# Optimization experiments

Hardware: AMD Instinct MI355X
Metric: run time of the kernel (lower is better)

## Reference

```python
import jax, jax.numpy as jnp
import numpy as np

N_RAYS = 65536
S_UNIFORM = 256          # 2 * n_samples coarse samples per ray
N_IMP = 128              # importance samples per ray
TRUNCATION = 2.0 / 512.0 * 4.0  # default in sdf2weights


def raw2weights_occupancy(raw):
    # raw2outputs_nerf_color with occupancy=True
    alpha = jax.nn.sigmoid(10.0 * raw)  # [N, S]
    trans = jnp.cumprod(
        jnp.concatenate([jnp.ones_like(alpha[:, :1]), 1.0 - alpha + 1e-10], axis=-1),
        axis=-1,
    )[:, :-1]
    return alpha, alpha * trans


def sample_pdf_det(bins, weights, n_samples):
    # bins: [N, M], weights: [N, M-1]; deterministic (det=True) inverse-CDF sampling
    w = weights + 1e-5
    pdf = w / jnp.sum(w, axis=-1, keepdims=True)
    cdf = jnp.cumsum(pdf, axis=-1)
    cdf = jnp.concatenate([jnp.zeros_like(cdf[..., :1]), cdf], axis=-1)  # [N, M]
    u = jnp.linspace(0.0, 1.0, n_samples, dtype=cdf.dtype)
    u = jnp.broadcast_to(u, cdf.shape[:-1] + (n_samples,))               # [N, n]
    inds = jax.vmap(lambda c, uu: jnp.searchsorted(c, uu, side='right'))(cdf, u)
    below = jnp.maximum(inds - 1, 0)
    above = jnp.minimum(inds, cdf.shape[-1] - 1)
    cdf_b = jnp.take_along_axis(cdf, below, axis=-1)
    cdf_a = jnp.take_along_axis(cdf, above, axis=-1)
    bins_b = jnp.take_along_axis(bins, below, axis=-1)
    bins_a = jnp.take_along_axis(bins, above, axis=-1)
    denom = cdf_a - cdf_b
    denom = jnp.where(denom < 1e-5, jnp.ones_like(denom), denom)
    t = (u - cdf_b) / denom
    return bins_b + t * (bins_a - bins_b)


def sdf2weights(sdf, z_vals, truncation=TRUNCATION, sc_factor=1.0):
    alpha = jax.nn.sigmoid(sdf / truncation) * jax.nn.sigmoid(-sdf / truncation)
    signs = sdf[:, 1:] * sdf[:, :-1]
    sign_mask = jnp.where(signs < 0.0, 1.0, 0.0)
    inds = jnp.argmax(sign_mask, axis=1)[:, None]              # first zero-crossing
    z_min = jnp.take_along_axis(z_vals, inds, axis=1)          # [N, 1]
    trunc_mask = jnp.where(z_vals < z_min + sc_factor * truncation, 1.0, 0.0)
    alpha = alpha * trunc_mask
    weights = alpha / (jnp.sum(alpha, axis=-1, keepdims=True) + 1e-8)
    return weights


def setup_inputs() -> dict:
    key = jax.random.key(0)
    k1, k2, k3, k4 = jax.random.split(key, 4)
    occ = jax.random.normal(k1, (N_RAYS, S_UNIFORM), dtype=jnp.float32)
    # monotonically increasing depths in [0.1, 4.1)
    z_vals_u = jnp.sort(
        jax.random.uniform(k2, (N_RAYS, S_UNIFORM), dtype=jnp.float32) * 4.0 + 0.1,
        axis=-1,
    )
    sdf = jax.random.normal(k3, (N_RAYS, N_IMP), dtype=jnp.float32) * 0.05
    rgbs = jax.random.uniform(k4, (N_RAYS, N_IMP, 3), dtype=jnp.float32)
    return {"occ": occ, "z_vals_u": z_vals_u, "sdf": sdf, "rgbs": rgbs}


def reference(occ, z_vals_u, sdf, rgbs):
    # 1) coarse occupancy compositing -> weights
    _, w_u = raw2weights_occupancy(occ)
    # 2) inverse-CDF importance sampling over midpoints (detached, as in gen_samples)
    z_mid = 0.5 * (z_vals_u[..., 1:] + z_vals_u[..., :-1])
    z_samples = jax.lax.stop_gradient(sample_pdf_det(z_mid, w_u[..., 1:-1], N_IMP))
    # 3) TSDF weights at importance samples
    weights = sdf2weights(sdf, z_samples)
    # 4) composite
    rgb_map = jnp.clip(jnp.sum(weights[..., None] * rgbs, axis=-2), 0.0, 1.0)  # [N,3]
    depth_map = jnp.sum(weights * z_samples, axis=-1)                          # [N]
    return jnp.concatenate([rgb_map, depth_map[:, None], weights], axis=-1)    # [N, 4+N_IMP]
```

## Files before the change

### kernel.cpp

```cpp
#include <hip/hip_runtime.h>

#define S_U 256
#define N_IMP 128
#define OUT_STRIDE (4 + N_IMP)
#define TRUNC 0.015625f
#define WPB 4

__device__ __forceinline__ float inv_cdf_sample(const float* __restrict__ cdf,
                                                const float* __restrict__ zm,
                                                float u) {
    int lo = 0, hi = 255;
#pragma unroll
    for (int it = 0; it < 8; ++it) {
        int mid = (lo + hi) >> 1;
        bool c = cdf[mid] <= u;
        lo = c ? mid + 1 : lo;
        hi = c ? hi : mid;
    }
    int below = max(lo - 1, 0);
    int above = min(lo, 254);
    float cb = cdf[below], ca = cdf[above];
    float zb = zm[below],  za = zm[above];
    float denom = ca - cb;
    denom = (denom < 1e-5f) ? 1.0f : denom;
    float t = (u - cb) / denom;
    return zb + t * (za - zb);
}

__global__ __launch_bounds__(256) void tsdf_render_kernel(
    const float* __restrict__ occ,
    const float* __restrict__ zvals,
    const float* __restrict__ sdf,
    const float* __restrict__ rgbs,
    float* __restrict__ out)
{
    const int lane = threadIdx.x & 63;
    const int wv   = threadIdx.x >> 6;
    const int ray  = blockIdx.x * WPB + wv;

    __shared__ __align__(16) float s_cdf [WPB][S_U];
    __shared__ __align__(16) float s_zmid[WPB][S_U];

    const float4 o4 = ((const float4*)(occ   + (size_t)ray * S_U))[lane];
    const float4 z4 = ((const float4*)(zvals + (size_t)ray * S_U))[lane];

    float a0 = 1.0f / (1.0f + __expf(-10.0f * o4.x));
    float a1 = 1.0f / (1.0f + __expf(-10.0f * o4.y));
    float a2 = 1.0f / (1.0f + __expf(-10.0f * o4.z));
    float a3 = 1.0f / (1.0f + __expf(-10.0f * o4.w));
    float t0 = 1.0f - a0 + 1e-10f;
    float t1 = 1.0f - a1 + 1e-10f;
    float t2 = 1.0f - a2 + 1e-10f;
    float t3 = 1.0f - a3 + 1e-10f;

    float pp0 = t0, pp1 = pp0 * t1, pp2 = pp1 * t2, pp3 = pp2 * t3;
    float ip = pp3;
#pragma unroll
    for (int d = 1; d < 64; d <<= 1) {
        float y = __shfl_up(ip, d);
        if (lane >= d) ip *= y;
    }
    float pbase = __shfl_up(ip, 1);
    if (lane == 0) pbase = 1.0f;

    float w0 = a0 * pbase;
    float w1 = a1 * pbase * pp0;
    float w2 = a2 * pbase * pp1;
    float w3 = a3 * pbase * pp2;

    float v0 = (lane > 0)  ? w0 + 1e-5f : 0.0f;
    float v1 = w1 + 1e-5f;
    float v2 = w2 + 1e-5f;
    float v3 = (lane < 63) ? w3 + 1e-5f : 0.0f;
    float s0 = v0, s1 = s0 + v1, s2 = s1 + v2, s3 = s2 + v3;
    float is = s3;
#pragma unroll
    for (int d = 1; d < 64; d <<= 1) {
        float y = __shfl_up(is, d);
        if (lane >= d) is += y;
    }
    float total = __shfl(is, 63);
    float sbase = __shfl_up(is, 1);
    if (lane == 0) sbase = 0.0f;
    float invt = 1.0f / total;

    float4 cdf4;
    cdf4.x = (sbase + s0) * invt;
    cdf4.y = (sbase + s1) * invt;
    cdf4.z = (sbase + s2) * invt;
    cdf4.w = (sbase + s3) * invt;
    *((float4*)&s_cdf[wv][lane * 4]) = cdf4;

    float znext = __shfl_down(z4.x, 1);
    float4 zm4;
    zm4.x = 0.5f * (z4.x + z4.y);
    zm4.y = 0.5f * (z4.y + z4.z);
    zm4.z = 0.5f * (z4.z + z4.w);
    zm4.w = 0.5f * (z4.w + znext);
    *((float4*)&s_zmid[wv][lane * 4]) = zm4;

    __builtin_amdgcn_wave_barrier();

    const float2 sd2 = ((const float2*)(sdf + (size_t)ray * N_IMP))[lane];
    const float2* rg = (const float2*)(rgbs + (size_t)ray * (N_IMP * 3)) + lane * 3;
    float2 p0 = rg[0];
    float2 p1 = rg[1];
    float2 p2 = rg[2];

    const float* cdfp = s_cdf[wv];
    const float* zmp  = s_zmid[wv];
    float u0 = (float)(2 * lane)     * (1.0f / 127.0f);
    float u1 = (float)(2 * lane + 1) * (1.0f / 127.0f);
    float zs0 = inv_cdf_sample(cdfp, zmp, u0);
    float zs1 = inv_cdf_sample(cdfp, zmp, u1);

    float sn = __shfl_down(sd2.x, 1);
    int c = 0x7fffffff;
    if (sd2.x * sd2.y < 0.0f)                     c = 2 * lane;
    else if (lane < 63 && sd2.y * sn < 0.0f)      c = 2 * lane + 1;
#pragma unroll
    for (int d = 32; d > 0; d >>= 1) c = min(c, __shfl_xor(c, d));
    int ci = (c == 0x7fffffff) ? 0 : c;
    float zca = __shfl(zs0, ci >> 1);
    float zcb = __shfl(zs1, ci >> 1);
    float z_min = (ci & 1) ? zcb : zca;

    float x0 = sd2.x * (1.0f / TRUNC);
    float x1 = sd2.y * (1.0f / TRUNC);
    float al0 = 1.0f / (2.0f + __expf(x0) + __expf(-x0));
    float al1 = 1.0f / (2.0f + __expf(x1) + __expf(-x1));
    float zlim = z_min + TRUNC;
    if (!(zs0 < zlim)) al0 = 0.0f;
    if (!(zs1 < zlim)) al1 = 0.0f;

    float asum = al0 + al1;
#pragma unroll
    for (int d = 32; d > 0; d >>= 1) asum += __shfl_xor(asum, d);
    float inv_s = 1.0f / (asum + 1e-8f);
    float g0 = al0 * inv_s;
    float g1 = al1 * inv_s;

    float rr = g0 * p0.x + g1 * p1.y;
    float gg = g0 * p0.y + g1 * p2.x;
    float bb = g0 * p1.x + g1 * p2.y;
    float dd = g0 * zs0  + g1 * zs1;
#pragma unroll
    for (int d = 32; d > 0; d >>= 1) {
        rr += __shfl_xor(rr, d);
        gg += __shfl_xor(gg, d);
        bb += __shfl_xor(bb, d);
        dd += __shfl_xor(dd, d);
    }

    float* ob = out + (size_t)ray * OUT_STRIDE;
    ((float2*)(ob + 4))[lane] = make_float2(g0, g1);
    if (lane == 0) {
        ob[0] = fminf(fmaxf(rr, 0.0f), 1.0f);
        ob[1] = fminf(fmaxf(gg, 0.0f), 1.0f);
        ob[2] = fminf(fmaxf(bb, 0.0f), 1.0f);
        ob[3] = dd;
    }
}

extern "C" void kernel_launch(void* const* d_in, const int* in_sizes, int n_in,
                              void* d_out, int out_size, void* d_ws, size_t ws_size,
                              hipStream_t stream) {
    const float* occ  = (const float*)d_in[0];
    const float* z    = (const float*)d_in[1];
    const float* sdf  = (const float*)d_in[2];
    const float* rgbs = (const float*)d_in[3];
    float* out = (float*)d_out;
    const int n_rays = in_sizes[0] / S_U;
    hipLaunchKernelGGL(tsdf_render_kernel, dim3(n_rays / WPB), dim3(256), 0, stream,
                       occ, z, sdf, rgbs, out);
}
```

Baseline: 263.6 us.

## Replace binary-search inverse CDF with scatter-based bucket lookup and DPP scans

Each lane computes which uniform sample indices its CDF entries bracket and scatters the 'below' index into shared memory. This replaces the per-sample 8-step binary search over LDS with a direct lookup. CDF and midpoint values are interleaved as float2 pairs so the below/above fetches pair up. Shuffle-based scans and reductions are replaced with DPP row operations. The colour and depth sums are reduced before normalisation, and the sdf/rgb loads are hoisted to the kernel start to overlap latency. The risks are the exactness of k_of at bucket boundaries and divergent scatter loops when the CDF is steep.

```diff
diff --git a/kernel.cpp b/kernel.cpp
--- a/kernel.cpp
+++ b/kernel.cpp
@@ -5,26 +5,51 @@
 #define OUT_STRIDE (4 + N_IMP)
 #define TRUNC 0.015625f
 #define WPB 4
+#define INV127 (1.0f / 127.0f)
 
-__device__ __forceinline__ float inv_cdf_sample(const float* __restrict__ cdf,
-                                                const float* __restrict__ zm,
-                                                float u) {
-    int lo = 0, hi = 255;
-#pragma unroll
-    for (int it = 0; it < 8; ++it) {
-        int mid = (lo + hi) >> 1;
-        bool c = cdf[mid] <= u;
-        lo = c ? mid + 1 : lo;
-        hi = c ? hi : mid;
-    }
-    int below = max(lo - 1, 0);
-    int above = min(lo, 254);
-    float cb = cdf[below], ca = cdf[above];
-    float zb = zm[below],  za = zm[above];
-    float denom = ca - cb;
-    denom = (denom < 1e-5f) ? 1.0f : denom;
-    float t = (u - cb) / denom;
-    return zb + t * (za - zb);
+template <int CTRL, int ROWM>
+__device__ __forceinline__ float dppf(float identity, float x) {
+    return __int_as_float(__builtin_amdgcn_update_dpp(
+        __float_as_int(identity), __float_as_int(x), CTRL, ROWM, 0xf, false));
+}
+
+__device__ __forceinline__ float wscan_add(float x) {
+    x += dppf<0x111, 0xf>(0.f, x);
+    x += dppf<0x112, 0xf>(0.f, x);
+    x += dppf<0x114, 0xf>(0.f, x);
+    x += dppf<0x118, 0xf>(0.f, x);
+    x += dppf<0x142, 0xa>(0.f, x);
+    x += dppf<0x143, 0xc>(0.f, x);
+    return x;
+}
+
+__device__ __forceinline__ float wscan_mul(float x) {
+    x *= dppf<0x111, 0xf>(1.f, x);
+    x *= dppf<0x112, 0xf>(1.f, x);
+    x *= dppf<0x114, 0xf>(1.f, x);
+    x *= dppf<0x118, 0xf>(1.f, x);
+    x *= dppf<0x142, 0xa>(1.f, x);
+    x *= dppf<0x143, 0xc>(1.f, x);
+    return x;
+}
+
+__device__ __forceinline__ int wscan_min(int x) {
+    const int I = 0x7fffffff;
+    x = min(x, __builtin_amdgcn_update_dpp(I, x, 0x111, 0xf, 0xf, false));
+    x = min(x, __builtin_amdgcn_update_dpp(I, x, 0x112, 0xf, 0xf, false));
+    x = min(x, __builtin_amdgcn_update_dpp(I, x, 0x114, 0xf, 0xf, false));
+    x = min(x, __builtin_amdgcn_update_dpp(I, x, 0x118, 0xf, 0xf, false));
+    x = min(x, __builtin_amdgcn_update_dpp(I, x, 0x142, 0xa, 0xf, false));
+    x = min(x, __builtin_amdgcn_update_dpp(I, x, 0x143, 0xc, 0xf, false));
+    return x;
+}
+
+__device__ __forceinline__ int k_of(float c) {
+    int k = (int)ceilf(c * 127.0f);
+    k = min(max(k, 0), 128);
+    if (k > 0 && c <= (float)(k - 1) * INV127) --k;
+    else if (k < 128 && !(c <= (float)k * INV127)) ++k;
+    return k;
 }
 
 __global__ __launch_bounds__(256) void tsdf_render_kernel(
@@ -38,11 +63,16 @@
     const int wv   = threadIdx.x >> 6;
     const int ray  = blockIdx.x * WPB + wv;
 
-    __shared__ __align__(16) float s_cdf [WPB][S_U];
-    __shared__ __align__(16) float s_zmid[WPB][S_U];
+    __shared__ __align__(16) float2 s_pair[WPB][S_U];
+    __shared__ int s_below[WPB][N_IMP];
 
     const float4 o4 = ((const float4*)(occ   + (size_t)ray * S_U))[lane];
     const float4 z4 = ((const float4*)(zvals + (size_t)ray * S_U))[lane];
+    const float2 sd2 = ((const float2*)(sdf + (size_t)ray * N_IMP))[lane];
+    const float2* rg = (const float2*)(rgbs + (size_t)ray * (N_IMP * 3)) + lane * 3;
+    const float2 p0 = rg[0];
+    const float2 p1 = rg[1];
+    const float2 p2 = rg[2];
 
     float a0 = 1.0f / (1.0f + __expf(-10.0f * o4.x));
     float a1 = 1.0f / (1.0f + __expf(-10.0f * o4.y));
@@ -52,14 +82,8 @@
     float t1 = 1.0f - a1 + 1e-10f;
     float t2 = 1.0f - a2 + 1e-10f;
     float t3 = 1.0f - a3 + 1e-10f;
-
     float pp0 = t0, pp1 = pp0 * t1, pp2 = pp1 * t2, pp3 = pp2 * t3;
-    float ip = pp3;
-#pragma unroll
-    for (int d = 1; d < 64; d <<= 1) {
-        float y = __shfl_up(ip, d);
-        if (lane >= d) ip *= y;
-    }
+    float ip = wscan_mul(pp3);
     float pbase = __shfl_up(ip, 1);
     if (lane == 0) pbase = 1.0f;
 
@@ -73,54 +97,60 @@
     float v2 = w2 + 1e-5f;
     float v3 = (lane < 63) ? w3 + 1e-5f : 0.0f;
     float s0 = v0, s1 = s0 + v1, s2 = s1 + v2, s3 = s2 + v3;
-    float is = s3;
-#pragma unroll
-    for (int d = 1; d < 64; d <<= 1) {
-        float y = __shfl_up(is, d);
-        if (lane >= d) is += y;
-    }
+    float is = wscan_add(s3);
     float total = __shfl(is, 63);
     float sbase = __shfl_up(is, 1);
     if (lane == 0) sbase = 0.0f;
     float invt = 1.0f / total;
 
-    float4 cdf4;
-    cdf4.x = (sbase + s0) * invt;
-    cdf4.y = (sbase + s1) * invt;
-    cdf4.z = (sbase + s2) * invt;
-    cdf4.w = (sbase + s3) * invt;
-    *((float4*)&s_cdf[wv][lane * 4]) = cdf4;
+    float c0 = (sbase + s0) * invt;
+    float c1 = (sbase + s1) * invt;
+    float c2 = (sbase + s2) * invt;
+    float c3 = (sbase + s3) * invt;
 
     float znext = __shfl_down(z4.x, 1);
-    float4 zm4;
-    zm4.x = 0.5f * (z4.x + z4.y);
-    zm4.y = 0.5f * (z4.y + z4.z);
-    zm4.z = 0.5f * (z4.z + z4.w);
-    zm4.w = 0.5f * (z4.w + znext);
-    *((float4*)&s_zmid[wv][lane * 4]) = zm4;
+    float zm0 = 0.5f * (z4.x + z4.y);
+    float zm1 = 0.5f * (z4.y + z4.z);
+    float zm2 = 0.5f * (z4.z + z4.w);
+    float zm3 = 0.5f * (z4.w + znext);
+
+    float2* pr = s_pair[wv];
+    *(float4*)&pr[lane * 4 + 0] = make_float4(c0, zm0, c1, zm1);
+    *(float4*)&pr[lane * 4 + 2] = make_float4(c2, zm2, c3, zm3);
+
+    int k0 = k_of(c0), k1 = k_of(c1), k2 = k_of(c2), k3 = k_of(c3);
+    int kn = __shfl_down(k0, 1);
+    if (lane == 63) { k3 = 128; kn = 128; }
+    int base = lane * 4;
+    int* bel = s_below[wv];
+    for (int j = k0; j < k1; ++j) bel[j] = base;
+    for (int j = k1; j < k2; ++j) bel[j] = base + 1;
+    for (int j = k2; j < k3; ++j) bel[j] = base + 2;
+    for (int j = k3; j < kn; ++j) bel[j] = base + 3;
 
     __builtin_amdgcn_wave_barrier();
 
-    const float2 sd2 = ((const float2*)(sdf + (size_t)ray * N_IMP))[lane];
-    const float2* rg = (const float2*)(rgbs + (size_t)ray * (N_IMP * 3)) + lane * 3;
-    float2 p0 = rg[0];
-    float2 p1 = rg[1];
-    float2 p2 = rg[2];
+    int jj0 = 2 * lane, jj1 = 2 * lane + 1;
+    int b0 = bel[jj0], b1 = bel[jj1];
+    float2 pb0 = pr[b0];
+    float2 pa0 = pr[min(b0 + 1, 254)];
+    float2 pb1 = pr[b1];
+    float2 pa1 = pr[min(b1 + 1, 254)];
 
-    const float* cdfp = s_cdf[wv];
-    const float* zmp  = s_zmid[wv];
-    float u0 = (float)(2 * lane)     * (1.0f / 127.0f);
-    float u1 = (float)(2 * lane + 1) * (1.0f / 127.0f);
-    float zs0 = inv_cdf_sample(cdfp, zmp, u0);
-    float zs1 = inv_cdf_sample(cdfp, zmp, u1);
+    float u0 = (float)jj0 * INV127;
+    float u1 = (float)jj1 * INV127;
+    float d0 = pa0.x - pb0.x; d0 = (d0 < 1e-5f) ? 1.0f : d0;
+    float d1 = pa1.x - pb1.x; d1 = (d1 < 1e-5f) ? 1.0f : d1;
+    float zs0 = pb0.y + ((u0 - pb0.x) / d0) * (pa0.y - pb0.y);
+    float zs1 = pb1.y + ((u1 - pb1.x) / d1) * (pa1.y - pb1.y);
 
     float sn = __shfl_down(sd2.x, 1);
     int c = 0x7fffffff;
-    if (sd2.x * sd2.y < 0.0f)                     c = 2 * lane;
-    else if (lane < 63 && sd2.y * sn < 0.0f)      c = 2 * lane + 1;
-#pragma unroll
-    for (int d = 32; d > 0; d >>= 1) c = min(c, __shfl_xor(c, d));
-    int ci = (c == 0x7fffffff) ? 0 : c;
+    if (sd2.x * sd2.y < 0.0f)                 c = 2 * lane;
+    else if (lane < 63 && sd2.y * sn < 0.0f)  c = 2 * lane + 1;
+    c = wscan_min(c);
+    int ci = __shfl(c, 63);
+    if (ci == 0x7fffffff) ci = 0;
     float zca = __shfl(zs0, ci >> 1);
     float zcb = __shfl(zs1, ci >> 1);
     float z_min = (ci & 1) ? zcb : zca;
@@ -133,32 +163,23 @@
     if (!(zs0 < zlim)) al0 = 0.0f;
     if (!(zs1 < zlim)) al1 = 0.0f;
 
-    float asum = al0 + al1;
-#pragma unroll
-    for (int d = 32; d > 0; d >>= 1) asum += __shfl_xor(asum, d);
+    float sA = wscan_add(al0 + al1);
+    float sR = wscan_add(al0 * p0.x + al1 * p1.y);
+    float sG = wscan_add(al0 * p0.y + al1 * p2.x);
+    float sB = wscan_add(al0 * p1.x + al1 * p2.y);
+    float sD = wscan_add(al0 * zs0  + al1 * zs1);
+
+    float asum = __shfl(sA, 63);
     float inv_s = 1.0f / (asum + 1e-8f);
-    float g0 = al0 * inv_s;
-    float g1 = al1 * inv_s;
-
-    float rr = g0 * p0.x + g1 * p1.y;
-    float gg = g0 * p0.y + g1 * p2.x;
-    float bb = g0 * p1.x + g1 * p2.y;
-    float dd = g0 * zs0  + g1 * zs1;
-#pragma unroll
-    for (int d = 32; d > 0; d >>= 1) {
-        rr += __shfl_xor(rr, d);
-        gg += __shfl_xor(gg, d);
-        bb += __shfl_xor(bb, d);
-        dd += __shfl_xor(dd, d);
-    }
 
     float* ob = out + (size_t)ray * OUT_STRIDE;
-    ((float2*)(ob + 4))[lane] = make_float2(g0, g1);
-    if (lane == 0) {
-        ob[0] = fminf(fmaxf(rr, 0.0f), 1.0f);
-        ob[1] = fminf(fmaxf(gg, 0.0f), 1.0f);
-        ob[2] = fminf(fmaxf(bb, 0.0f), 1.0f);
-        ob[3] = dd;
+    ((float2*)(ob + 4))[lane] = make_float2(al0 * inv_s, al1 * inv_s);
+    if (lane == 63) {
+        float inv63 = 1.0f / (sA + 1e-8f);
+        ob[0] = fminf(fmaxf(sR * inv63, 0.0f), 1.0f);
+        ob[1] = fminf(fmaxf(sG * inv63, 0.0f), 1.0f);
+        ob[2] = fminf(fmaxf(sB * inv63, 0.0f), 1.0f);
+        ob[3] = sD * inv63;
     }
 }
 
```

Result: slower. 269.4 us (+2.2%).
